# Kernel tuning notes

Hardware: AMD Instinct MI355X
Metric: run time of the kernel (lower is better)

The kernel has to match this reference:

```python
import jax, jax.numpy as jnp
import numpy as np

B, RES, DIM, H, KD = 16, 32, 768, 12, 64
N = RES * RES          # 1024 tokens
D = KD                 # attn_ratio = 1 -> per-head value dim == key_dim
DH = D * H             # 768
SCALE = KD ** -0.5
LN_EPS = 1e-5


def _bias_idxs():
    # replicate the itertools.product construction: for row-major points,
    # offsets (|dy|,|dx|) are first seen in order dy-major, so id = |dy|*RES + |dx|
    coords = np.arange(N)
    y, x = coords // RES, coords % RES
    dy = np.abs(y[:, None] - y[None, :])
    dx = np.abs(x[:, None] - x[None, :])
    return jnp.asarray(dy * RES + dx, dtype=jnp.int32)  # [N, N]


def setup_inputs() -> dict:
    key = jax.random.key(0)
    ks = jax.random.split(key, 8)
    return {
        "x": jax.random.normal(ks[0], (B, N, DIM), jnp.float32),
        "ln_w": 1.0 + 0.01 * jax.random.normal(ks[1], (DIM,), jnp.float32),
        "ln_b": 0.01 * jax.random.normal(ks[2], (DIM,), jnp.float32),
        "qkv_w": 0.02 * jax.random.normal(ks[3], (3 * H * KD, DIM), jnp.float32),
        "qkv_b": 0.01 * jax.random.normal(ks[4], (3 * H * KD,), jnp.float32),
        "proj_w": 0.02 * jax.random.normal(ks[5], (DIM, DH), jnp.float32),
        "proj_b": 0.01 * jax.random.normal(ks[6], (DIM,), jnp.float32),
        "attn_biases": 0.1 * jax.random.normal(ks[7], (H, RES * RES), jnp.float32),
        "bias_idxs": _bias_idxs(),
    }


def reference(x, ln_w, ln_b, qkv_w, qkv_b, proj_w, proj_b, attn_biases, bias_idxs):
    # LayerNorm over the feature dim
    mu = jnp.mean(x, axis=-1, keepdims=True)
    var = jnp.mean(jnp.square(x - mu), axis=-1, keepdims=True)
    xn = (x - mu) * jax.lax.rsqrt(var + LN_EPS) * ln_w + ln_b

    # fused qkv projection -> [B, N, H, 3*KD], split per head
    qkv = (xn @ qkv_w.T + qkv_b).reshape(B, N, H, 3 * KD)
    q, k, v = jnp.split(qkv, [KD, 2 * KD], axis=3)  # each [B, N, H, KD]

    # gathered relative-position bias: [H, N, N]
    bias = attn_biases[:, bias_idxs]

    # scores + bias -> softmax -> AV
    attn = jnp.einsum("bnhk,bmhk->bhnm", q, k) * SCALE + bias[None]
    attn = jax.nn.softmax(attn, axis=-1)
    out = jnp.einsum("bhnm,bmhd->bnhd", attn, v).reshape(B, N, DH)
    return out @ proj_w.T + proj_b
```

## Files before the change

kernel.cpp:

```cpp
#include <hip/hip_runtime.h>
#include <cstdint>
#include <cstddef>

#define AS1 __attribute__((address_space(1)))
#define AS3 __attribute__((address_space(3)))

typedef float f32x4 __attribute__((ext_vector_type(4)));
typedef __bf16 bf16x8 __attribute__((ext_vector_type(8)));
typedef __bf16 bf16x4 __attribute__((ext_vector_type(4)));
typedef _Float16 h16x4 __attribute__((ext_vector_type(4)));
typedef uint32_t u32x4 __attribute__((ext_vector_type(4)));

__device__ __forceinline__ void async_cp16(void* lds, const void* g) {
    __builtin_amdgcn_global_load_lds((AS1 void*)(g), (AS3 void*)(lds), 16, 0, 0);
}

__device__ __forceinline__ bf16x8 frag_of(u32x4 u) {
    return __builtin_bit_cast(bf16x8, u);
}

__global__ __launch_bounds__(256)
void cvt_w(const float* __restrict__ qkvw, const float* __restrict__ projw,
           __bf16* __restrict__ qkvwb, __bf16* __restrict__ projwb) {
    int i = blockIdx.x * 256 + threadIdx.x;
    if (i < 442368) {
        int row = i / 192, c4 = (i - row * 192) * 4;
        int t = (row >= 1536) ? 2 : (row >= 768 ? 1 : 0);
        int rem = row - t * 768;
        int hh = rem >> 6, d = rem & 63;
        int in_row = hh * 192 + t * 64 + d;
        float4 v = *(const float4*)(qkvw + (long)in_row * 768 + c4);
        bf16x4 o;
        o[0] = (__bf16)v.x; o[1] = (__bf16)v.y; o[2] = (__bf16)v.z; o[3] = (__bf16)v.w;
        *(bf16x4*)(qkvwb + (long)row * 768 + c4) = o;
    } else {
        int j = i - 442368;
        float4 v = ((const float4*)projw)[j];
        bf16x4 o;
        o[0] = (__bf16)v.x; o[1] = (__bf16)v.y; o[2] = (__bf16)v.z; o[3] = (__bf16)v.w;
        ((bf16x4*)projwb)[j] = o;
    }
}

__global__ __launch_bounds__(256)
void ln_kernel(const float* __restrict__ x, const float* __restrict__ w,
               const float* __restrict__ bsh, __bf16* __restrict__ xn) {
    const int lane = threadIdx.x & 63;
    const long row = (long)blockIdx.x * 4 + (threadIdx.x >> 6);
    const float4* xr = (const float4*)(x + row * 768);
    float4 v[3];
    v[0] = xr[lane]; v[1] = xr[lane + 64]; v[2] = xr[lane + 128];
    float s = 0.f, ss = 0.f;
#pragma unroll
    for (int i = 0; i < 3; ++i) {
        s  += v[i].x + v[i].y + v[i].z + v[i].w;
        ss += v[i].x * v[i].x + v[i].y * v[i].y + v[i].z * v[i].z + v[i].w * v[i].w;
    }
#pragma unroll
    for (int m = 1; m < 64; m <<= 1) { s += __shfl_xor(s, m); ss += __shfl_xor(ss, m); }
    const float mean = s * (1.f / 768.f);
    const float rstd = rsqrtf(ss * (1.f / 768.f) - mean * mean + 1e-5f);
    const float4* wv = (const float4*)w;
    const float4* bv = (const float4*)bsh;
    bf16x4* outp = (bf16x4*)(xn + row * 768);
#pragma unroll
    for (int i = 0; i < 3; ++i) {
        float4 wi = wv[lane + 64 * i], bi = bv[lane + 64 * i];
        bf16x4 o;
        o[0] = (__bf16)((v[i].x - mean) * rstd * wi.x + bi.x);
        o[1] = (__bf16)((v[i].y - mean) * rstd * wi.y + bi.y);
        o[2] = (__bf16)((v[i].z - mean) * rstd * wi.z + bi.z);
        o[3] = (__bf16)((v[i].w - mean) * rstd * wi.w + bi.w);
        outp[lane + 64 * i] = o;
    }
}

template <int SWAP>
__device__ __forceinline__
void gemm256_body(char* smem, const __bf16* __restrict__ A,
                  const __bf16* __restrict__ Bw, const float* __restrict__ bias,
                  __bf16* __restrict__ q_out, __bf16* __restrict__ k_out,
                  __bf16* __restrict__ vt_out, long bm, long bn) {
    const int tid  = threadIdx.x;
    const int lane = tid & 63;
    const int quad = lane >> 4;
    const int l16  = lane & 15;
    const int wave = tid >> 6;
    const int wm = wave >> 2, wn = wave & 3;

    const __bf16* Ag = A  + bm * 768;
    const __bf16* Bg = Bw + bn * 768;
    const int r0  = tid >> 2;
    const int sc  = ((tid & 3) ^ ((tid >> 3) & 3)) * 8;
    const int swq = quad ^ ((l16 >> 1) & 3);

    f32x4 acc[8][4] = {};

    auto stage = [&](int t) {
        char* base = smem + (size_t)(t & 3) * 32768;
        const __bf16* As_ = Ag + t * 32 + sc;
        const __bf16* Bs_ = Bg + t * 32 + sc;
        async_cp16(base + tid * 16,                 As_ + (size_t)r0 * 768);
        async_cp16(base + (tid + 512) * 16,         As_ + (size_t)(r0 + 128) * 768);
        async_cp16(base + 16384 + tid * 16,         Bs_ + (size_t)r0 * 768);
        async_cp16(base + 16384 + (tid + 512) * 16, Bs_ + (size_t)(r0 + 128) * 768);
    };

    auto kstep = [&](int buf) {
        const u32x4* Ab = (const u32x4*)(smem + (size_t)buf * 32768);
        const u32x4* Bb = (const u32x4*)(smem + (size_t)buf * 32768 + 16384);
        bf16x8 af[8], bfv[4];
#pragma unroll
        for (int m = 0; m < 8; ++m)
            af[m] = frag_of(Ab[(wm * 128 + m * 16 + l16) * 4 + swq]);
#pragma unroll
        for (int n = 0; n < 4; ++n)
            bfv[n] = frag_of(Bb[(wn * 64 + n * 16 + l16) * 4 + swq]);
        __builtin_amdgcn_s_setprio(1);
#pragma unroll
        for (int m = 0; m < 8; ++m)
#pragma unroll
            for (int n = 0; n < 4; ++n) {
                if constexpr (SWAP)
                    acc[m][n] = __builtin_amdgcn_mfma_f32_16x16x32_bf16(bfv[n], af[m], acc[m][n], 0, 0, 0);
                else
                    acc[m][n] = __builtin_amdgcn_mfma_f32_16x16x32_bf16(af[m], bfv[n], acc[m][n], 0, 0, 0);
            }
        __builtin_amdgcn_s_setprio(0);
    };

    stage(0); stage(1); stage(2);
    for (int t = 0; t < 21; ++t) {
        asm volatile("s_waitcnt vmcnt(8)" ::: "memory");
        __builtin_amdgcn_s_barrier();
        stage(t + 3);
        kstep(t & 3);
    }
    asm volatile("s_waitcnt vmcnt(8)" ::: "memory");
    __builtin_amdgcn_s_barrier();
    kstep(1);
    asm volatile("s_waitcnt vmcnt(4)" ::: "memory");
    __builtin_amdgcn_s_barrier();
    kstep(2);
    asm volatile("s_waitcnt vmcnt(0)" ::: "memory");
    __builtin_amdgcn_s_barrier();
    kstep(3);

    if constexpr (SWAP) {
#pragma unroll
        for (int n = 0; n < 4; ++n) {
            int col0 = (int)bn + wn * 64 + n * 16 + quad * 4;
            int t_ = col0 >= 768;
            int cc = col0 - t_ * 768;
            int hh = cc >> 6, dd = cc & 63;
            int f  = hh * 192 + t_ * 64 + dd;
            float4 bb = *(const float4*)(bias + f);
            __bf16* dst = t_ ? k_out : q_out;
#pragma unroll
            for (int m = 0; m < 8; ++m) {
                long row = bm + wm * 128 + m * 16 + l16;
                long b   = row >> 10;
                long nn  = row & 1023;
                bf16x4 pk;
                pk[0] = (__bf16)(acc[m][n][0] + bb.x);
                pk[1] = (__bf16)(acc[m][n][1] + bb.y);
                pk[2] = (__bf16)(acc[m][n][2] + bb.z);
                pk[3] = (__bf16)(acc[m][n][3] + bb.w);
                *(bf16x4*)(dst + ((b * 12 + hh) * 1024 + nn) * 64 + dd) = pk;
            }
        }
    } else {
#pragma unroll
        for (int n = 0; n < 4; ++n) {
            int cv = (int)bn - 1536 + wn * 64 + n * 16 + l16;
            int hh = cv >> 6, dd = cv & 63;
            float bv = bias[hh * 192 + 128 + dd];
#pragma unroll
            for (int m = 0; m < 8; ++m) {
                long row0 = bm + wm * 128 + m * 16 + quad * 4;
                long b    = row0 >> 10;
                long n0   = row0 & 1023;
                bf16x4 pk;
                pk[0] = (__bf16)(acc[m][n][0] + bv);
                pk[1] = (__bf16)(acc[m][n][1] + bv);
                pk[2] = (__bf16)(acc[m][n][2] + bv);
                pk[3] = (__bf16)(acc[m][n][3] + bv);
                *(bf16x4*)(vt_out + ((b * 12 + hh) * 64 + dd) * 1024 + n0) = pk;
            }
        }
    }
}

__global__ __launch_bounds__(512, 2)
void gemm_qkv(const __bf16* __restrict__ A, const __bf16* __restrict__ Bw,
              const float* __restrict__ bias, __bf16* __restrict__ qb,
              __bf16* __restrict__ kb, __bf16* __restrict__ vtb) {
    extern __shared__ char smem[];
    int blk  = blockIdx.x;
    int xcd  = blk & 7;
    int rest = blk >> 3;
    int bx   = rest % 9;
    int byg  = rest / 9;
    long by  = xcd + 8 * byg;
    long bm  = by * 256, bn = (long)bx * 256;
    if (bx < 6)
        gemm256_body<1>(smem, A, Bw, bias, qb, kb, nullptr, bm, bn);
    else
        gemm256_body<0>(smem, A, Bw, bias, nullptr, nullptr, vtb, bm, bn);
}

__device__ __forceinline__
void gemm_core1(__bf16* As, __bf16* Bs,
                const __bf16* __restrict__ A, const __bf16* __restrict__ Bw,
                const float* __restrict__ bias, float* __restrict__ f_out,
                long bm, long bn) {
    constexpr int K = 768;
    const int tid  = threadIdx.x;
    const int lane = tid & 63;
    const int quad = lane >> 4;
    const int l16  = lane & 15;
    const int wave = tid >> 6;
    const int wm = wave >> 1, wn = wave & 1;

    const __bf16* Ab = A  + bm * K;
    const __bf16* Bb = Bw + bn * K;

    const int el0 = tid, el1 = tid + 256;
    const int rA0 = el0 >> 2, rA1 = el1 >> 2;
    const int kc  = (tid & 3) * 8;

    f32x4 acc[4][4] = {};

    for (int k0 = 0; k0 < K; k0 += 32) {
        __syncthreads();
        async_cp16((char*)As + el0 * 16, Ab + (long)rA0 * K + (k0 + kc));
        async_cp16((char*)As + el1 * 16, Ab + (long)rA1 * K + (k0 + kc));
        async_cp16((char*)Bs + el0 * 16, Bb + (long)rA0 * K + (k0 + kc));
        async_cp16((char*)Bs + el1 * 16, Bb + (long)rA1 * K + (k0 + kc));
        __syncthreads();

        const u32x4* Av = (const u32x4*)As;
        const u32x4* Bv = (const u32x4*)Bs;
        bf16x8 af[4], bfr[4];
#pragma unroll
        for (int t = 0; t < 4; ++t) {
            af[t]  = frag_of(Av[(wm * 64 + t * 16 + l16) * 4 + quad]);
            bfr[t] = frag_of(Bv[(wn * 64 + t * 16 + l16) * 4 + quad]);
        }
#pragma unroll
        for (int i = 0; i < 4; ++i)
#pragma unroll
            for (int j = 0; j < 4; ++j)
                acc[i][j] = __builtin_amdgcn_mfma_f32_16x16x32_bf16(af[i], bfr[j], acc[i][j], 0, 0, 0);
    }

#pragma unroll
    for (int i = 0; i < 4; ++i) {
#pragma unroll
        for (int r = 0; r < 4; ++r) {
            long row = bm + wm * 64 + i * 16 + quad * 4 + r;
#pragma unroll
            for (int j = 0; j < 4; ++j) {
                int col = (int)bn + wn * 64 + j * 16 + l16;
                f_out[row * 768 + col] = acc[i][j][r] + bias[col];
            }
        }
    }
}

__global__ __launch_bounds__(256, 3)
void gemm_proj(const __bf16* __restrict__ A, const __bf16* __restrict__ Bw,
               const float* __restrict__ bias, float* __restrict__ out) {
    __shared__ __align__(16) __bf16 As[128 * 32];
    __shared__ __align__(16) __bf16 Bs[128 * 32];
    int blk  = blockIdx.x;
    int xcd  = blk & 7;
    int rest = blk >> 3;
    int bx   = rest % 6;
    int byg  = rest / 6;
    long by  = xcd + 8 * byg;
    gemm_core1(As, Bs, A, Bw, bias, out, by * 128, (long)bx * 128);
}

__global__ __launch_bounds__(512, 6)
void attn_kernel(const __bf16* __restrict__ Q, const __bf16* __restrict__ Kb,
                 const __bf16* __restrict__ Vt, const float* __restrict__ biases,
                 __bf16* __restrict__ out) {
    __shared__ __align__(16) __bf16 QPs[128 * 64];
    __shared__ __align__(16) __bf16 Ks[2][64 * 64];
    __shared__ __align__(16) __bf16 Vts[2][64 * 64];
    __shared__ __align__(16) float brow[1024];

    const int tid  = threadIdx.x;
    const int lane = tid & 63;
    const int wave = tid >> 6;
    const int quad = lane >> 4;
    const int l16  = lane & 15;
    const int sw   = l16 & 7;

    int blk  = blockIdx.x;
    int xcd  = blk & 7;
    int rest = blk >> 3;
    int qt   = rest & 7;
    int bhg  = rest >> 3;
    int bh_i = xcd + 8 * bhg;
    int b    = bh_i / 12;
    int h    = bh_i - b * 12;

    const long bh = bh_i;
    const __bf16* Qg  = Q  + (bh * 1024 + qt * 128) * 64;
    const __bf16* Kg  = Kb + bh * 1024 * 64;
    const __bf16* Vtg = Vt + bh * 64 * 1024;

    {
        const int e0 = tid, e1 = tid + 512;
        const int r0 = e0 >> 3, c0 = (e0 & 7) ^ (r0 & 7);
        const int r1 = e1 >> 3, c1 = (e1 & 7) ^ (r1 & 7);
        async_cp16((char*)QPs + e0 * 16, Qg + r0 * 64 + c0 * 8);
        async_cp16((char*)QPs + e1 * 16, Qg + r1 * 64 + c1 * 8);
    }
    const int rk = tid >> 3;
    const int ck = (tid & 7) ^ (rk & 7);
    async_cp16((char*)Ks[0]  + tid * 16, Kg  + rk * 64   + ck * 8);
    async_cp16((char*)Vts[0] + tid * 16, Vtg + rk * 1024 + ck * 8);
    {
        const float LOG2E = 1.4426950408889634f;
        float2 v = ((const float2*)(biases + (long)h * 1024))[tid];
        float2 o; o.x = v.x * LOG2E; o.y = v.y * LOG2E;
        *(float2*)(brow + tid * 2) = o;
    }
    __syncthreads();

    bf16x8 aq[2];
    {
        const u32x4* Qv = (const u32x4*)QPs;
        int qrow = wave * 16 + l16;
        aq[0] = frag_of(Qv[qrow * 8 + (quad ^ sw)]);
        aq[1] = frag_of(Qv[qrow * 8 + ((quad + 4) ^ sw)]);
    }

    const int yq = 4 * qt + (wave >> 1);
    const int xq = ((wave & 1) << 4) + l16;
    int pdx[2][4];
#pragma unroll
    for (int i2 = 0; i2 < 2; ++i2)
#pragma unroll
        for (int r = 0; r < 4; ++r) {
            int xk = (i2 << 4) + quad * 4 + r;
            int d = xq - xk; pdx[i2][r] = d < 0 ? -d : d;
        }

    const float SSCALE = 0.125f * 1.4426950408889634f;
    float lacc = 0.f;
    f32x4 o[4] = {};
    __bf16* Psw = QPs + wave * 1024;
    const int pwb = l16 * 128 + (quad & 1) * 8;

    for (int kt = 0; kt < 16; ++kt) {
        const int cb = kt & 1;
        if (kt < 15) {
            const int nb = cb ^ 1;
            const __bf16* Kt  = Kg  + (kt + 1) * 4096;
            const __bf16* Vtt = Vtg + (kt + 1) * 64;
            async_cp16((char*)Ks[nb]  + tid * 16, Kt  + rk * 64   + ck * 8);
            async_cp16((char*)Vts[nb] + tid * 16, Vtt + rk * 1024 + ck * 8);
        }

        f32x4 s[4];
        const u32x4* Kv = (const u32x4*)Ks[cb];
#pragma unroll
        for (int nt = 0; nt < 4; ++nt) {
            int krow = nt * 16 + l16;
            bf16x8 k0 = frag_of(Kv[krow * 8 + (quad ^ sw)]);
            bf16x8 k1 = frag_of(Kv[krow * 8 + ((quad + 4) ^ sw)]);
            f32x4 z = {0.f, 0.f, 0.f, 0.f};
            z = __builtin_amdgcn_mfma_f32_16x16x32_bf16(k0, aq[0], z, 0, 0, 0);
            z = __builtin_amdgcn_mfma_f32_16x16x32_bf16(k1, aq[1], z, 0, 0, 0);
            s[nt] = z;
        }

        int dy0 = yq - 2 * kt;     dy0 = dy0 < 0 ? -dy0 : dy0;
        int dy1 = yq - 2 * kt - 1; dy1 = dy1 < 0 ? -dy1 : dy1;
        const float* br0 = brow + dy0 * 32;
        const float* br1 = brow + dy1 * 32;
#pragma unroll
        for (int nt = 0; nt < 4; ++nt) {
            const float* br = (nt & 2) ? br1 : br0;
            bf16x4 pk;
#pragma unroll
            for (int r = 0; r < 4; ++r) {
                float p = __builtin_amdgcn_exp2f(s[nt][r] * SSCALE + br[pdx[nt & 1][r]]);
                lacc += p;
                pk[r] = (__bf16)p;
            }
            *(bf16x4*)((char*)Psw + pwb + (((nt * 2 + (quad >> 1)) ^ sw) << 4)) = pk;
        }

        const u32x4* Pv = (const u32x4*)Psw;
        const u32x4* Vv = (const u32x4*)Vts[cb];
        bf16x8 bp0 = frag_of(Pv[l16 * 8 + (quad ^ sw)]);
        bf16x8 bp1 = frag_of(Pv[l16 * 8 + ((quad + 4) ^ sw)]);
#pragma unroll
        for (int dt = 0; dt < 4; ++dt) {
            int vrow = dt * 16 + l16;
            bf16x8 v0 = frag_of(Vv[vrow * 8 + (quad ^ sw)]);
            bf16x8 v1 = frag_of(Vv[vrow * 8 + ((quad + 4) ^ sw)]);
            o[dt] = __builtin_amdgcn_mfma_f32_16x16x32_bf16(v0, bp0, o[dt], 0, 0, 0);
            o[dt] = __builtin_amdgcn_mfma_f32_16x16x32_bf16(v1, bp1, o[dt], 0, 0, 0);
        }

        __syncthreads();
    }

    lacc += __shfl_xor(lacc, 16);
    lacc += __shfl_xor(lacc, 32);
    const float rl = 1.f / lacc;

    const long n = qt * 128 + wave * 16 + l16;
    __bf16* op = out + ((long)b * 1024 + n) * 768 + h * 64 + quad * 4;
#pragma unroll
    for (int dt = 0; dt < 4; ++dt) {
        bf16x4 ov;
        ov[0] = (__bf16)(o[dt][0] * rl);
        ov[1] = (__bf16)(o[dt][1] * rl);
        ov[2] = (__bf16)(o[dt][2] * rl);
        ov[3] = (__bf16)(o[dt][3] * rl);
        *(bf16x4*)(op + dt * 16) = ov;
    }
}

extern "C" void kernel_launch(void* const* d_in, const int* in_sizes, int n_in,
                              void* d_out, int out_size, void* d_ws, size_t ws_size,
                              hipStream_t stream) {
    (void)in_sizes; (void)n_in; (void)out_size; (void)ws_size;
    const float* x      = (const float*)d_in[0];
    const float* ln_w   = (const float*)d_in[1];
    const float* ln_b   = (const float*)d_in[2];
    const float* qkv_w  = (const float*)d_in[3];
    const float* qkv_b  = (const float*)d_in[4];
    const float* proj_w = (const float*)d_in[5];
    const float* proj_b = (const float*)d_in[6];
    const float* ab     = (const float*)d_in[7];
    float* outp = (float*)d_out;

    char* ws = (char*)d_ws;
    __bf16* xn     = (__bf16*)(ws);
    __bf16* aout   = (__bf16*)(ws);
    __bf16* qkvwb  = (__bf16*)(ws + 25165824);
    __bf16* projwb = (__bf16*)(ws + 28704768);
    __bf16* qb     = (__bf16*)(ws + 29884416);
    __bf16* kb     = (__bf16*)(ws + 55050240);
    __bf16* vtb    = (__bf16*)(ws + 80216064);

    cvt_w<<<2304, 256, 0, stream>>>(qkv_w, proj_w, qkvwb, projwb);
    ln_kernel<<<4096, 256, 0, stream>>>(x, ln_w, ln_b, xn);
    gemm_qkv<<<576, 512, 131072, stream>>>(xn, qkvwb, qkv_b, qb, kb, vtb);
    attn_kernel<<<1536, 512, 0, stream>>>(qb, kb, vtb, ab, aout);
    gemm_proj<<<768, 256, 0, stream>>>(aout, projwb, proj_b, outp);
}
```

Baseline: 323.2 us.

## Process two 16-row query groups per wave in attention, halving block threads

The attention kernel now runs 4 waves of 256 threads instead of 8, and each wave handles 32 query rows as two 16-row groups. Each K and V fragment read from LDS is reused across both groups, which cuts LDS traffic per MFMA. Cooperative loads now issue twice as many async copies per thread. In exchange, register pressure roughly doubles for accumulators and scores, and there are fewer waves per block to hide latency. The launch bounds are relaxed to match.

```diff
diff --git a/kernel.cpp b/kernel.cpp
--- a/kernel.cpp
+++ b/kernel.cpp
@@ -282,7 +282,7 @@
     gemm_core1(As, Bs, A, Bw, bias, out, by * 128, (long)bx * 128);
 }
 
-__global__ __launch_bounds__(512, 6)
+__global__ __launch_bounds__(256, 3)
 void attn_kernel(const __bf16* __restrict__ Q, const __bf16* __restrict__ Kb,
                  const __bf16* __restrict__ Vt, const float* __restrict__ biases,
                  __bf16* __restrict__ out) {
@@ -312,49 +312,56 @@
     const __bf16* Kg  = Kb + bh * 1024 * 64;
     const __bf16* Vtg = Vt + bh * 64 * 1024;
 
-    {
-        const int e0 = tid, e1 = tid + 512;
-        const int r0 = e0 >> 3, c0 = (e0 & 7) ^ (r0 & 7);
-        const int r1 = e1 >> 3, c1 = (e1 & 7) ^ (r1 & 7);
-        async_cp16((char*)QPs + e0 * 16, Qg + r0 * 64 + c0 * 8);
-        async_cp16((char*)QPs + e1 * 16, Qg + r1 * 64 + c1 * 8);
+#pragma unroll
+    for (int j = 0; j < 4; ++j) {
+        int e = tid + 256 * j;
+        int r = e >> 3, c = (e & 7) ^ (r & 7);
+        async_cp16((char*)QPs + e * 16, Qg + r * 64 + c * 8);
     }
     const int rk = tid >> 3;
     const int ck = (tid & 7) ^ (rk & 7);
-    async_cp16((char*)Ks[0]  + tid * 16, Kg  + rk * 64   + ck * 8);
-    async_cp16((char*)Vts[0] + tid * 16, Vtg + rk * 1024 + ck * 8);
+    async_cp16((char*)Ks[0]  + tid * 16,         Kg  + rk * 64 + ck * 8);
+    async_cp16((char*)Ks[0]  + (tid + 256) * 16, Kg  + (rk + 32) * 64 + ck * 8);
+    async_cp16((char*)Vts[0] + tid * 16,         Vtg + rk * 1024 + ck * 8);
+    async_cp16((char*)Vts[0] + (tid + 256) * 16, Vtg + (rk + 32) * 1024 + ck * 8);
     {
         const float LOG2E = 1.4426950408889634f;
-        float2 v = ((const float2*)(biases + (long)h * 1024))[tid];
-        float2 o; o.x = v.x * LOG2E; o.y = v.y * LOG2E;
-        *(float2*)(brow + tid * 2) = o;
+        float4 v = ((const float4*)(biases + (long)h * 1024))[tid];
+        float4 o; o.x = v.x * LOG2E; o.y = v.y * LOG2E;
+        o.z = v.z * LOG2E; o.w = v.w * LOG2E;
+        *(float4*)(brow + tid * 4) = o;
     }
     __syncthreads();
 
-    bf16x8 aq[2];
+    bf16x8 aq[2][2];
     {
         const u32x4* Qv = (const u32x4*)QPs;
-        int qrow = wave * 16 + l16;
-        aq[0] = frag_of(Qv[qrow * 8 + (quad ^ sw)]);
-        aq[1] = frag_of(Qv[qrow * 8 + ((quad + 4) ^ sw)]);
-    }
-
-    const int yq = 4 * qt + (wave >> 1);
-    const int xq = ((wave & 1) << 4) + l16;
-    int pdx[2][4];
-#pragma unroll
-    for (int i2 = 0; i2 < 2; ++i2)
-#pragma unroll
-        for (int r = 0; r < 4; ++r) {
-            int xk = (i2 << 4) + quad * 4 + r;
-            int d = xq - xk; pdx[i2][r] = d < 0 ? -d : d;
-        }
+#pragma unroll
+        for (int g = 0; g < 2; ++g) {
+            int qrow = wave * 32 + g * 16 + l16;
+            aq[g][0] = frag_of(Qv[qrow * 8 + (quad ^ sw)]);
+            aq[g][1] = frag_of(Qv[qrow * 8 + ((quad + 4) ^ sw)]);
+        }
+    }
+
+    const int yq = 4 * qt + wave;
+    int pdx[2][2][4];
+#pragma unroll
+    for (int g = 0; g < 2; ++g)
+#pragma unroll
+        for (int i2 = 0; i2 < 2; ++i2)
+#pragma unroll
+            for (int r = 0; r < 4; ++r) {
+                int xk = (i2 << 4) + quad * 4 + r;
+                int d = (g * 16 + l16) - xk; pdx[g][i2][r] = d < 0 ? -d : d;
+            }
 
     const float SSCALE = 0.125f * 1.4426950408889634f;
-    float lacc = 0.f;
-    f32x4 o[4] = {};
-    __bf16* Psw = QPs + wave * 1024;
-    const int pwb = l16 * 128 + (quad & 1) * 8;
+    float lacc[2] = {0.f, 0.f};
+    f32x4 o[2][4] = {};
+    __bf16* Psw = QPs + wave * 2048;
+    const int pwb0 = l16 * 128 + (quad & 1) * 8;
+    const int pwb1 = pwb0 + 2048;
 
     for (int kt = 0; kt < 16; ++kt) {
         const int cb = kt & 1;
@@ -362,21 +369,26 @@
             const int nb = cb ^ 1;
             const __bf16* Kt  = Kg  + (kt + 1) * 4096;
             const __bf16* Vtt = Vtg + (kt + 1) * 64;
-            async_cp16((char*)Ks[nb]  + tid * 16, Kt  + rk * 64   + ck * 8);
-            async_cp16((char*)Vts[nb] + tid * 16, Vtt + rk * 1024 + ck * 8);
-        }
-
-        f32x4 s[4];
+            async_cp16((char*)Ks[nb]  + tid * 16,         Kt  + rk * 64 + ck * 8);
+            async_cp16((char*)Ks[nb]  + (tid + 256) * 16, Kt  + (rk + 32) * 64 + ck * 8);
+            async_cp16((char*)Vts[nb] + tid * 16,         Vtt + rk * 1024 + ck * 8);
+            async_cp16((char*)Vts[nb] + (tid + 256) * 16, Vtt + (rk + 32) * 1024 + ck * 8);
+        }
+
+        f32x4 s[2][4];
         const u32x4* Kv = (const u32x4*)Ks[cb];
 #pragma unroll
         for (int nt = 0; nt < 4; ++nt) {
             int krow = nt * 16 + l16;
             bf16x8 k0 = frag_of(Kv[krow * 8 + (quad ^ sw)]);
             bf16x8 k1 = frag_of(Kv[krow * 8 + ((quad + 4) ^ sw)]);
-            f32x4 z = {0.f, 0.f, 0.f, 0.f};
-            z = __builtin_amdgcn_mfma_f32_16x16x32_bf16(k0, aq[0], z, 0, 0, 0);
-            z = __builtin_amdgcn_mfma_f32_16x16x32_bf16(k1, aq[1], z, 0, 0, 0);
-            s[nt] = z;
+#pragma unroll
+            for (int g = 0; g < 2; ++g) {
+                f32x4 z = {0.f, 0.f, 0.f, 0.f};
+                z = __builtin_amdgcn_mfma_f32_16x16x32_bf16(k0, aq[g][0], z, 0, 0, 0);
+                z = __builtin_amdgcn_mfma_f32_16x16x32_bf16(k1, aq[g][1], z, 0, 0, 0);
+                s[g][nt] = z;
+            }
         }
 
         int dy0 = yq - 2 * kt;     dy0 = dy0 < 0 ? -dy0 : dy0;
@@ -384,48 +396,63 @@
         const float* br0 = brow + dy0 * 32;
         const float* br1 = brow + dy1 * 32;
 #pragma unroll
-        for (int nt = 0; nt < 4; ++nt) {
-            const float* br = (nt & 2) ? br1 : br0;
-            bf16x4 pk;
-#pragma unroll
-            for (int r = 0; r < 4; ++r) {
-                float p = __builtin_amdgcn_exp2f(s[nt][r] * SSCALE + br[pdx[nt & 1][r]]);
-                lacc += p;
-                pk[r] = (__bf16)p;
-            }
-            *(bf16x4*)((char*)Psw + pwb + (((nt * 2 + (quad >> 1)) ^ sw) << 4)) = pk;
+        for (int g = 0; g < 2; ++g) {
+            const int pwb = g ? pwb1 : pwb0;
+#pragma unroll
+            for (int nt = 0; nt < 4; ++nt) {
+                const float* br = (nt & 2) ? br1 : br0;
+                bf16x4 pk;
+#pragma unroll
+                for (int r = 0; r < 4; ++r) {
+                    float p = __builtin_amdgcn_exp2f(s[g][nt][r] * SSCALE + br[pdx[g][nt & 1][r]]);
+                    lacc[g] += p;
+                    pk[r] = (__bf16)p;
+                }
+                *(bf16x4*)((char*)Psw + pwb + (((nt * 2 + (quad >> 1)) ^ sw) << 4)) = pk;
+            }
         }
 
         const u32x4* Pv = (const u32x4*)Psw;
         const u32x4* Vv = (const u32x4*)Vts[cb];
-        bf16x8 bp0 = frag_of(Pv[l16 * 8 + (quad ^ sw)]);
-        bf16x8 bp1 = frag_of(Pv[l16 * 8 + ((quad + 4) ^ sw)]);
+        bf16x8 bp[2][2];
+#pragma unroll
+        for (int g = 0; g < 2; ++g) {
+            int prow = g * 16 + l16;
+            bp[g][0] = frag_of(Pv[prow * 8 + (quad ^ sw)]);
+            bp[g][1] = frag_of(Pv[prow * 8 + ((quad + 4) ^ sw)]);
+        }
 #pragma unroll
         for (int dt = 0; dt < 4; ++dt) {
             int vrow = dt * 16 + l16;
             bf16x8 v0 = frag_of(Vv[vrow * 8 + (quad ^ sw)]);
             bf16x8 v1 = frag_of(Vv[vrow * 8 + ((quad + 4) ^ sw)]);
-            o[dt] = __builtin_amdgcn_mfma_f32_16x16x32_bf16(v0, bp0, o[dt], 0, 0, 0);
-            o[dt] = __builtin_amdgcn_mfma_f32_16x16x32_bf16(v1, bp1, o[dt], 0, 0, 0);
+#pragma unroll
+            for (int g = 0; g < 2; ++g) {
+                o[g][dt] = __builtin_amdgcn_mfma_f32_16x16x32_bf16(v0, bp[g][0], o[g][dt], 0, 0, 0);
+                o[g][dt] = __builtin_amdgcn_mfma_f32_16x16x32_bf16(v1, bp[g][1], o[g][dt], 0, 0, 0);
+            }
         }
 
         __syncthreads();
     }
 
-    lacc += __shfl_xor(lacc, 16);
-    lacc += __shfl_xor(lacc, 32);
-    const float rl = 1.f / lacc;
-
-    const long n = qt * 128 + wave * 16 + l16;
-    __bf16* op = out + ((long)b * 1024 + n) * 768 + h * 64 + quad * 4;
-#pragma unroll
-    for (int dt = 0; dt < 4; ++dt) {
-        bf16x4 ov;
-        ov[0] = (__bf16)(o[dt][0] * rl);
-        ov[1] = (__bf16)(o[dt][1] * rl);
-        ov[2] = (__bf16)(o[dt][2] * rl);
-        ov[3] = (__bf16)(o[dt][3] * rl);
-        *(bf16x4*)(op + dt * 16) = ov;
+#pragma unroll
+    for (int g = 0; g < 2; ++g) {
+        float la = lacc[g];
+        la += __shfl_xor(la, 16);
+        la += __shfl_xor(la, 32);
+        const float rl = 1.f / la;
+        const long n = qt * 128 + wave * 32 + g * 16 + l16;
+        __bf16* op = out + ((long)b * 1024 + n) * 768 + h * 64 + quad * 4;
+#pragma unroll
+        for (int dt = 0; dt < 4; ++dt) {
+            bf16x4 ov;
+            ov[0] = (__bf16)(o[g][dt][0] * rl);
+            ov[1] = (__bf16)(o[g][dt][1] * rl);
+            ov[2] = (__bf16)(o[g][dt][2] * rl);
+            ov[3] = (__bf16)(o[g][dt][3] * rl);
+            *(bf16x4*)(op + dt * 16) = ov;
+        }
     }
 }
 
@@ -455,6 +482,6 @@
     cvt_w<<<2304, 256, 0, stream>>>(qkv_w, proj_w, qkvwb, projwb);
     ln_kernel<<<4096, 256, 0, stream>>>(x, ln_w, ln_b, xn);
     gemm_qkv<<<576, 512, 131072, stream>>>(xn, qkvwb, qkv_b, qb, kb, vtb);
-    attn_kernel<<<1536, 512, 0, stream>>>(qb, kb, vtb, ab, aout);
+    attn_kernel<<<1536, 256, 0, stream>>>(qb, kb, vtb, ab, aout);
     gemm_proj<<<768, 256, 0, stream>>>(aout, projwb, proj_b, outp);
 }
```

New measurement: 317.3 us. Within noise of the previous version (-1.8%).
